# Kernel tuning notes

Hardware: AMD Instinct MI355X
Metric: run time of the kernel (lower is better)

Reference implementation:

```python
import jax, jax.numpy as jnp
import numpy as np

N_POWER_ITERS = 10  # torch spectral_norm power-iteration approximation of sigma_max

def _spectral_normalize(W):
    # Power iteration for largest singular value; u, v are treated as constants
    # w.r.t. gradients (matches torch.nn.utils.parametrizations.spectral_norm).
    u = jnp.ones((W.shape[0],), W.dtype) / jnp.sqrt(jnp.asarray(W.shape[0], W.dtype))
    def body(u, _):
        v = W.T @ u
        v = v / (jnp.linalg.norm(v) + 1e-12)
        u = W @ v
        u = u / (jnp.linalg.norm(u) + 1e-12)
        return u, None
    u, _ = jax.lax.scan(body, u, None, length=N_POWER_ITERS)
    u = jax.lax.stop_gradient(u)
    v = W.T @ u
    v = jax.lax.stop_gradient(v / (jnp.linalg.norm(v) + 1e-12))
    sigma = u @ (W @ v)
    return W / sigma

def setup_inputs() -> dict:
    key = jax.random.key(0)
    k1, k2, k3, k4 = jax.random.split(key, 4)
    B, T, D_in, H, D_out = 32, 1024, 1024, 1024, 1024
    x = jax.random.normal(k1, (B, T, D_in), dtype=jnp.float32)
    # nn.Linear weight shape: [out_features, in_features]
    W_A = jax.random.normal(k2, (H, H), dtype=jnp.float32) * (1.0 / np.sqrt(H))
    W_B = jax.random.normal(k3, (H, D_in), dtype=jnp.float32) * (1.0 / np.sqrt(D_in))
    W_C = jax.random.normal(k4, (D_out, H), dtype=jnp.float32) * (1.0 / np.sqrt(H))
    return {"x": x, "W_A": W_A, "W_B": W_B, "W_C": W_C}

def reference(x, W_A, W_B, W_C):
    A = _spectral_normalize(W_A)   # [H, H]
    Bw = _spectral_normalize(W_B)  # [H, D_in]
    C = _spectral_normalize(W_C)   # [D_out, H]
    # Precompute input projection for all timesteps: [B, T, H]
    xb = jnp.einsum('bti,hi->bth', x, Bw)
    h0 = jnp.zeros((x.shape[0], A.shape[0]), x.dtype)
    def step(h, xb_t):
        h = h @ A.T + xb_t   # h_t = A h_{t-1} + B x_t
        return h, h
    _, hs = jax.lax.scan(step, h0, jnp.swapaxes(xb, 0, 1))  # [T, B, H]
    hs = jnp.swapaxes(hs, 0, 1)                              # [B, T, H]
    ys = jnp.einsum('bth,oh->bto', hs, C)                    # y_t = C h_t
    return ys, hs
```

## Files before the change

kernel.cpp:

```cpp
#include <hip/hip_runtime.h>
#include <hip/hip_fp16.h>
#include <stdint.h>
#include <math.h>


typedef unsigned short us;
typedef float  floatx4 __attribute__((ext_vector_type(4)));
typedef short  shortx8 __attribute__((ext_vector_type(8)));

#define HDIM 1024
#define MALL 32768

__device__ __forceinline__ us f2bf(float f) {
  union { float f; unsigned u; } v; v.f = f;
  unsigned u = v.u;
  return (us)((u + 0x7FFFu + ((u >> 16) & 1u)) >> 16);
}
__device__ __forceinline__ float bf2f(us h) {
  union { float f; unsigned u; } v; v.u = ((unsigned)h) << 16;
  return v.f;
}

__device__ __forceinline__ void gbar(int* bar, int idx) {
  __threadfence();
  __syncthreads();
  if (threadIdx.x == 0) {
    __hip_atomic_fetch_add(&bar[idx], 1, __ATOMIC_ACQ_REL, __HIP_MEMORY_SCOPE_AGENT);
    while (__hip_atomic_load(&bar[idx], __ATOMIC_ACQUIRE, __HIP_MEMORY_SCOPE_AGENT) < 8)
      __builtin_amdgcn_s_sleep(2);
  }
  __syncthreads();
}

__global__ void k_power(const float* __restrict__ WA, const float* __restrict__ WB,
                        const float* __restrict__ WC,
                        float* __restrict__ uu, float* __restrict__ vv,
                        float* __restrict__ rsig, int* __restrict__ bar) {
  const int m = blockIdx.y, b = blockIdx.x, tid = threadIdx.x;
  const float* W = m == 0 ? WA : (m == 1 ? WB : WC);
  float* um = uu + m * 1024;
  float* vm = vv + m * 1024;
  int* barm = bar + m * 32;
  __shared__ float red[1024];
  __shared__ float vs[1024];

  if (tid < 128) um[b * 128 + tid] = 0.03125f;
  gbar(barm, 0);

  auto ssq_of = [&](const float* p) -> float {
    float a = p[tid];
    red[tid] = a * a; __syncthreads();
    for (int o = 512; o > 0; o >>= 1) { if (tid < o) red[tid] += red[tid + o]; __syncthreads(); }
    float r = red[0]; __syncthreads();
    return r;
  };

  const int il = tid & 127, jp = tid >> 7;
  const int jr = tid >> 3, ip = tid & 7;

  for (int it = 0; it <= 10; ++it) {
    float su = rsqrtf(ssq_of(um) + 1e-24f);
    {
      int i = b * 128 + il;
      float acc = 0.f;
      const float* Wp = W + (size_t)(jp * 128) * 1024 + i;
      #pragma unroll 4
      for (int j = 0; j < 128; ++j) acc = fmaf(Wp[(size_t)j * 1024], um[jp * 128 + j], acc);
      red[tid] = acc; __syncthreads();
      if (tid < 128) {
        float s = red[il] + red[il + 128] + red[il + 256] + red[il + 384]
                + red[il + 512] + red[il + 640] + red[il + 768] + red[il + 896];
        vm[b * 128 + il] = s * su;
      }
      __syncthreads();
    }
    gbar(barm, 1 + 2 * it);
    if (it == 10) break;
    float sv = rsqrtf(ssq_of(vm) + 1e-24f);
    vs[tid] = vm[tid] * sv;
    __syncthreads();
    {
      int j = b * 128 + jr;
      const float* Wr = W + (size_t)j * 1024;
      float acc = 0.f;
      #pragma unroll 4
      for (int k = 0; k < 128; ++k) acc = fmaf(Wr[ip + 8 * k], vs[ip + 8 * k], acc);
      #pragma unroll
      for (int o = 4; o > 0; o >>= 1) acc += __shfl_down(acc, o, 8);
      if (ip == 0) um[j] = acc;
    }
    __syncthreads();
    gbar(barm, 2 + 2 * it);
  }
  if (b == 0) {
    float s = ssq_of(vm);
    if (tid == 0) rsig[m] = rsqrtf(s + 1e-24f);
  }
}

__global__ void k_cast_mats(const float* __restrict__ WA, const float* __restrict__ WB,
                            const float* __restrict__ WC, const float* __restrict__ rsig,
                            us* __restrict__ dst) {
  int idx = blockIdx.x * 256 + threadIdx.x;
  if (idx >= 786432) return;
  int m = idx >> 18;
  const float* W = m == 0 ? WA : (m == 1 ? WB : WC);
  float rs = rsig[m];
  float4 v = ((const float4*)W)[idx & 262143];
  unsigned lo = f2bf(v.x * rs) | ((unsigned)f2bf(v.y * rs) << 16);
  unsigned hi = f2bf(v.z * rs) | ((unsigned)f2bf(v.w * rs) << 16);
  ((uint2*)dst)[idx] = make_uint2(lo, hi);
}

__global__ void k_cast_x(const float* __restrict__ src, us* __restrict__ dst, int n4) {
  int idx = blockIdx.x * 256 + threadIdx.x;
  int stride = gridDim.x * 256;
  for (; idx < n4; idx += stride) {
    float4 v = ((const float4*)src)[idx];
    unsigned lo = f2bf(v.x) | ((unsigned)f2bf(v.y) << 16);
    unsigned hi = f2bf(v.z) | ((unsigned)f2bf(v.w) << 16);
    ((uint2*)dst)[idx] = make_uint2(lo, hi);
  }
}

__global__ void k_transpose(const us* __restrict__ src, us* __restrict__ dst) {
  __shared__ us t[32][33];
  int bx = blockIdx.x * 32, by = blockIdx.y * 32;
  int tx = threadIdx.x & 31, ty = threadIdx.x >> 5;
  for (int r = ty; r < 32; r += 8)
    t[r][tx] = src[(size_t)(by + r) * 1024 + bx + tx];
  __syncthreads();
  for (int r = ty; r < 32; r += 8)
    dst[(size_t)(bx + r) * 1024 + by + tx] = t[tx][r];
}

template <int TILE>
__global__ __launch_bounds__(256, 3)
void k_gemm(const us* __restrict__ Abf, const us* __restrict__ Bmat,
            const us* __restrict__ AccP,
            float* __restrict__ Out32, us* __restrict__ Out16, us* __restrict__ OutH,
            us* __restrict__ Copy16,
            int M, int stride_log, int delta_a, int delta_acc, int delta_copy,
            int accmode, int zero_aop) {
  constexpr int BK = 64;
  constexpr int WT = TILE / 2;
  constexpr int NT = WT / 16;
  constexpr int QA = TILE / 32;

  __shared__ us ldsA[TILE * BK];
  __shared__ us ldsB[TILE * BK];

  const int tid = threadIdx.x;
  const int wave = tid >> 6, lane = tid & 63;
  const int wr = wave >> 1, wc = wave & 1;
  const int lr = lane & 15, g = lane >> 4;
  const int m0 = blockIdx.x * TILE, n0 = blockIdx.y * TILE;

  const int cnt_log = 10 - stride_log;
  const int cnt_mask = (1 << cnt_log) - 1;
  auto rowC = [&](int m) -> int {
    int j = m & cnt_mask, b = m >> cnt_log;
    return (b << 10) + (((j + 1) << stride_log) - 1);
  };

  floatx4 acc[NT][NT];
  if (accmode == 0) {
    #pragma unroll
    for (int i = 0; i < NT; ++i)
      #pragma unroll
      for (int j = 0; j < NT; ++j) acc[i][j] = (floatx4)(0.0f);
  } else {
    #pragma unroll
    for (int ii = 0; ii < NT; ++ii) {
      #pragma unroll
      for (int r = 0; r < 4; ++r) {
        int m = m0 + wr * WT + ii * 16 + g * 4 + r;
        if (m >= M) m = M - 1;
        size_t rowoff = (size_t)(rowC(m) - delta_acc) * HDIM;
        #pragma unroll
        for (int jj = 0; jj < NT; ++jj) {
          int col = n0 + wc * WT + jj * 16 + lr;
          us raw = AccP[rowoff + col];
          acc[ii][jj][r] = (accmode == 2) ? bf2f(raw)
                                          : __half2float(*(const __half*)&raw);
        }
      }
    }
  }

  if (!zero_aop) {
    size_t abase[QA], bbase[QA];
    #pragma unroll
    for (int q = 0; q < QA; ++q) {
      int ch = tid + q * 256;
      int i = ch >> 3;
      int c = (ch & 7) ^ ((i >> 1) & 7);
      int m = m0 + i; if (m >= M) m = M - 1;
      abase[q] = (size_t)(rowC(m) - delta_a) * HDIM + c * 8;
      bbase[q] = (size_t)(n0 + i) * HDIM + c * 8;
    }
    for (int k0 = 0; k0 < HDIM; k0 += BK) {
      __syncthreads();
      #pragma unroll
      for (int q = 0; q < QA; ++q) {
        __builtin_amdgcn_global_load_lds(
            (const __attribute__((address_space(1))) void*)(Abf + abase[q] + k0),
            (__attribute__((address_space(3))) void*)(ldsA + (wave * 64 + q * 256) * 8),
            16, 0, 0);
        __builtin_amdgcn_global_load_lds(
            (const __attribute__((address_space(1))) void*)(Bmat + bbase[q] + k0),
            (__attribute__((address_space(3))) void*)(ldsB + (wave * 64 + q * 256) * 8),
            16, 0, 0);
      }
      __syncthreads();
      #pragma unroll
      for (int kk = 0; kk < 2; ++kk) {
        shortx8 af[NT], bfv[NT];
        #pragma unroll
        for (int ii = 0; ii < NT; ++ii) {
          int ra = wr * WT + ii * 16 + lr;
          af[ii] = *(const shortx8*)(ldsA + ra * BK + (((kk * 4 + g) ^ ((ra >> 1) & 7)) * 8));
          int rb = wc * WT + ii * 16 + lr;
          bfv[ii] = *(const shortx8*)(ldsB + rb * BK + (((kk * 4 + g) ^ ((rb >> 1) & 7)) * 8));
        }
        #pragma unroll
        for (int ii = 0; ii < NT; ++ii)
          #pragma unroll
          for (int jj = 0; jj < NT; ++jj)
            acc[ii][jj] = __builtin_amdgcn_mfma_f32_16x16x32_bf16(af[ii], bfv[jj], acc[ii][jj], 0, 0, 0);
      }
    }
  }

  #pragma unroll
  for (int ii = 0; ii < NT; ++ii) {
    #pragma unroll
    for (int r = 0; r < 4; ++r) {
      int m = m0 + wr * WT + ii * 16 + g * 4 + r;
      if (m >= M) continue;
      size_t rowoff = (size_t)rowC(m) * HDIM;
      #pragma unroll
      for (int jj = 0; jj < NT; ++jj) {
        int col = n0 + wc * WT + jj * 16 + lr;
        float v = acc[ii][jj][r];
        if (Copy16) {
          us pv = zero_aop ? (us)0 : Abf[rowoff + col];
          Copy16[(size_t)(rowC(m) - delta_copy) * HDIM + col] = pv;
        }
        if (Out32) Out32[rowoff + col] = v;
        if (Out16) Out16[rowoff + col] = f2bf(v);
        if (OutH) {
          __half hv = __float2half(v);
          OutH[rowoff + col] = *(const us*)&hv;
        }
      }
    }
  }
}

extern "C" void kernel_launch(void* const* d_in, const int* in_sizes, int n_in,
                              void* d_out, int out_size, void* d_ws, size_t ws_size,
                              hipStream_t stream) {
  const float* x  = (const float*)d_in[0];
  const float* WA = (const float*)d_in[1];
  const float* WB = (const float*)d_in[2];
  const float* WC = (const float*)d_in[3];

  float* ys = (float*)d_out;
  float* U  = ys + (size_t)MALL * HDIM;
  us* U16 = (us*)U;

  char* wsb = (char*)d_ws;
  int*   bar  = (int*)(wsb);
  float* rsig = (float*)(wsb + 2048);
  float* uu   = (float*)(wsb + 4096);
  float* vv   = (float*)(wsb + 20480);
  us* An = (us*)(wsb + 65536);
  us* Bn = An + 1048576;
  us* Cn = Bn + 1048576;
  us* PT = Cn + 1048576;
  us* Ppow[9];
  Ppow[0] = An;
  for (int d = 1; d <= 8; ++d) Ppow[d] = PT + (size_t)d * 1048576;
  us* Xbf  = (us*)(wsb + 25231360);
  us* Uh   = Xbf;
  us* U0bf = Xbf + (size_t)MALL * HDIM;
  us* Ubf  = U0bf + (size_t)MALL * HDIM;
  if (ws_size < 226643968ULL) return;

  auto gemm = [&](int tile, const us* A, const us* B, const us* accP,
                  float* o32, us* o16, us* oH, us* cp16,
                  int M, int slog, int da, int dacc, int dcp, int am, int za) {
    dim3 grid((M + tile - 1) / tile, HDIM / tile);
    if (tile == 128)
      k_gemm<128><<<grid, 256, 0, stream>>>(A, B, accP, o32, o16, oH, cp16, M, slog, da, dacc, dcp, am, za);
    else
      k_gemm<64><<<grid, 256, 0, stream>>>(A, B, accP, o32, o16, oH, cp16, M, slog, da, dacc, dcp, am, za);
  };

  hipMemsetAsync(bar, 0, 3 * 32 * sizeof(int), stream);
  k_power<<<dim3(8, 3), 1024, 0, stream>>>(WA, WB, WC, uu, vv, rsig, bar);

  k_cast_mats<<<dim3(3072), 256, 0, stream>>>(WA, WB, WC, rsig, An);
  k_cast_x<<<dim3(8192), 256, 0, stream>>>(x, Xbf, 8388608);

  for (int d = 1; d <= 8; ++d) {
    k_transpose<<<dim3(32, 32), 256, 0, stream>>>(Ppow[d - 1], PT);
    gemm(64, Ppow[d - 1], PT, nullptr, nullptr, Ppow[d], nullptr, nullptr,
         1024, 0, 0, 0, 0, 0, 0);
  }

  gemm(128, Xbf, Bn, nullptr, nullptr, U0bf, nullptr, nullptr, MALL, 0, 0, 0, 0, 0, 0);

  for (int d = 0; d <= 8; ++d) {
    int M = MALL >> (d + 1);
    const us* srcA = (d == 0) ? U0bf : Ubf;
    const us* accP = (d == 0) ? U0bf : Uh;
    int am = (d == 0) ? 2 : 3;
    gemm(M >= 2048 ? 128 : 64, srcA, Ppow[d], accP, nullptr, Ubf, Uh, nullptr,
         M, d + 1, 1 << d, 0, 0, am, 0);
  }

  {
    us* PP2[2] = {U16, Ubf};
    for (int idx = 0; idx <= 9; ++idx) {
      int d = 9 - idx;
      int M = MALL >> (d + 1);
      const us* srcA = idx ? PP2[(idx - 1) & 1] : nullptr;
      us* dst = PP2[idx & 1];
      const us* accP = (d == 0) ? U0bf : Uh;
      int am = (d == 0) ? 2 : 3;
      gemm(M >= 2048 ? 128 : 64, srcA, Ppow[d], accP,
           nullptr, dst, nullptr, dst,
           M, d + 1, 0, 1 << d, 1 << d, am, idx == 0 ? 1 : 0);
    }
  }

  gemm(128, Ubf, An, U0bf, U, U0bf, nullptr, nullptr, MALL, 0, 0, 0, 0, 2, 0);

  gemm(128, U0bf, Cn, nullptr, ys, nullptr, nullptr, nullptr, MALL, 0, 0, 0, 0, 0, 0);
}
```

Before: 1.553 ms.

## Spread power iteration over more blocks with partial-norm reductions

```diff
diff --git a/kernel.cpp b/kernel.cpp
--- a/kernel.cpp
+++ b/kernel.cpp
@@ -10,6 +10,7 @@
 
 #define HDIM 1024
 #define MALL 32768
+#define PNB  32
 
 __device__ __forceinline__ us f2bf(float f) {
   union { float f; unsigned u; } v; v.f = f;
@@ -19,6 +20,12 @@
 __device__ __forceinline__ float bf2f(us h) {
   union { float f; unsigned u; } v; v.u = ((unsigned)h) << 16;
   return v.f;
+}
+
+__device__ __forceinline__ float bsum32(float t) {
+  #pragma unroll
+  for (int o = 16; o > 0; o >>= 1) t += __shfl_xor(t, o, 32);
+  return t;
 }
 
 __device__ __forceinline__ void gbar(int* bar, int idx) {
@@ -26,7 +33,7 @@
   __syncthreads();
   if (threadIdx.x == 0) {
     __hip_atomic_fetch_add(&bar[idx], 1, __ATOMIC_ACQ_REL, __HIP_MEMORY_SCOPE_AGENT);
-    while (__hip_atomic_load(&bar[idx], __ATOMIC_ACQUIRE, __HIP_MEMORY_SCOPE_AGENT) < 8)
+    while (__hip_atomic_load(&bar[idx], __ATOMIC_ACQUIRE, __HIP_MEMORY_SCOPE_AGENT) < PNB)
       __builtin_amdgcn_s_sleep(2);
   }
   __syncthreads();
@@ -35,77 +42,124 @@
 __global__ void k_power(const float* __restrict__ WA, const float* __restrict__ WB,
                         const float* __restrict__ WC,
                         float* __restrict__ uu, float* __restrict__ vv,
-                        float* __restrict__ rsig, int* __restrict__ bar) {
+                        float* __restrict__ part, int* __restrict__ bar) {
   const int m = blockIdx.y, b = blockIdx.x, tid = threadIdx.x;
   const float* W = m == 0 ? WA : (m == 1 ? WB : WC);
   float* um = uu + m * 1024;
   float* vm = vv + m * 1024;
-  int* barm = bar + m * 32;
-  __shared__ float red[1024];
-  __shared__ float vs[1024];
-
-  if (tid < 128) um[b * 128 + tid] = 0.03125f;
-  gbar(barm, 0);
-
-  auto ssq_of = [&](const float* p) -> float {
-    float a = p[tid];
-    red[tid] = a * a; __syncthreads();
-    for (int o = 512; o > 0; o >>= 1) { if (tid < o) red[tid] += red[tid + o]; __syncthreads(); }
-    float r = red[0]; __syncthreads();
-    return r;
-  };
-
-  const int il = tid & 127, jp = tid >> 7;
-  const int jr = tid >> 3, ip = tid & 7;
+  float* PV = part + m * 1024;
+  float* PU = part + m * 1024 + 512;
+  int* barm = bar + m * 64;
+
+  __shared__ __align__(16) float sh[1024];
+  __shared__ __align__(16) float red[512];
+  __shared__ float bc;
+
+  const int il = tid & 31, jp = tid >> 5;
+  const int jr = tid >> 4, ip = tid & 15;
 
   for (int it = 0; it <= 10; ++it) {
-    float su = rsqrtf(ssq_of(um) + 1e-24f);
+    if (it == 0) {
+      ((float2*)sh)[tid] = make_float2(0.03125f, 0.03125f);
+      __syncthreads();
+    } else {
+      if (tid < 32) {
+        float t = bsum32(PU[(it - 1) * 32 + tid]);
+        if (tid == 0) bc = rsqrtf(t + 1e-24f);
+      }
+      __syncthreads();
+      float su = bc;
+      float2 u2 = ((const float2*)um)[tid];
+      ((float2*)sh)[tid] = make_float2(u2.x * su, u2.y * su);
+      __syncthreads();
+    }
+
     {
-      int i = b * 128 + il;
-      float acc = 0.f;
-      const float* Wp = W + (size_t)(jp * 128) * 1024 + i;
-      #pragma unroll 4
-      for (int j = 0; j < 128; ++j) acc = fmaf(Wp[(size_t)j * 1024], um[jp * 128 + j], acc);
-      red[tid] = acc; __syncthreads();
-      if (tid < 128) {
-        float s = red[il] + red[il + 128] + red[il + 256] + red[il + 384]
-                + red[il + 512] + red[il + 640] + red[il + 768] + red[il + 896];
-        vm[b * 128 + il] = s * su;
-      }
-      __syncthreads();
-    }
-    gbar(barm, 1 + 2 * it);
+      const int col = b * 32 + il;
+      const float* Wp = W + (size_t)(jp * 64) * 1024 + col;
+      const float* up = sh + jp * 64;
+      float a0 = 0.f, a1 = 0.f, a2 = 0.f, a3 = 0.f, a4 = 0.f, a5 = 0.f, a6 = 0.f, a7 = 0.f;
+      #pragma unroll
+      for (int j = 0; j < 64; j += 8) {
+        a0 = fmaf(Wp[(size_t)(j + 0) * 1024], up[j + 0], a0);
+        a1 = fmaf(Wp[(size_t)(j + 1) * 1024], up[j + 1], a1);
+        a2 = fmaf(Wp[(size_t)(j + 2) * 1024], up[j + 2], a2);
+        a3 = fmaf(Wp[(size_t)(j + 3) * 1024], up[j + 3], a3);
+        a4 = fmaf(Wp[(size_t)(j + 4) * 1024], up[j + 4], a4);
+        a5 = fmaf(Wp[(size_t)(j + 5) * 1024], up[j + 5], a5);
+        a6 = fmaf(Wp[(size_t)(j + 6) * 1024], up[j + 6], a6);
+        a7 = fmaf(Wp[(size_t)(j + 7) * 1024], up[j + 7], a7);
+      }
+      red[tid] = ((a0 + a1) + (a2 + a3)) + ((a4 + a5) + (a6 + a7));
+      __syncthreads();
+      if (tid < 32) {
+        float s = 0.f;
+        #pragma unroll
+        for (int g = 0; g < 16; ++g) s += red[tid + 32 * g];
+        vm[b * 32 + tid] = s;
+        float t = bsum32(s * s);
+        if (tid == 0) PV[it * 32 + b] = t;
+      }
+    }
     if (it == 10) break;
-    float sv = rsqrtf(ssq_of(vm) + 1e-24f);
-    vs[tid] = vm[tid] * sv;
+    gbar(barm, 2 * it);
+
+    if (tid < 32) {
+      float t = bsum32(PV[it * 32 + tid]);
+      if (tid == 0) bc = rsqrtf(t + 1e-24f);
+    }
     __syncthreads();
     {
-      int j = b * 128 + jr;
-      const float* Wr = W + (size_t)j * 1024;
-      float acc = 0.f;
-      #pragma unroll 4
-      for (int k = 0; k < 128; ++k) acc = fmaf(Wr[ip + 8 * k], vs[ip + 8 * k], acc);
-      #pragma unroll
-      for (int o = 4; o > 0; o >>= 1) acc += __shfl_down(acc, o, 8);
-      if (ip == 0) um[j] = acc;
+      float sv = bc;
+      float2 v2 = ((const float2*)vm)[tid];
+      ((float2*)sh)[tid] = make_float2(v2.x * sv, v2.y * sv);
     }
     __syncthreads();
-    gbar(barm, 2 + 2 * it);
-  }
-  if (b == 0) {
-    float s = ssq_of(vm);
-    if (tid == 0) rsig[m] = rsqrtf(s + 1e-24f);
+
+    {
+      const int row = b * 32 + jr;
+      const float* Wr = W + (size_t)row * 1024;
+      float b0 = 0.f, b1 = 0.f, b2 = 0.f, b3 = 0.f, b4 = 0.f, b5 = 0.f, b6 = 0.f, b7 = 0.f;
+      #pragma unroll
+      for (int k = 0; k < 64; k += 8) {
+        b0 = fmaf(Wr[ip + 16 * (k + 0)], sh[ip + 16 * (k + 0)], b0);
+        b1 = fmaf(Wr[ip + 16 * (k + 1)], sh[ip + 16 * (k + 1)], b1);
+        b2 = fmaf(Wr[ip + 16 * (k + 2)], sh[ip + 16 * (k + 2)], b2);
+        b3 = fmaf(Wr[ip + 16 * (k + 3)], sh[ip + 16 * (k + 3)], b3);
+        b4 = fmaf(Wr[ip + 16 * (k + 4)], sh[ip + 16 * (k + 4)], b4);
+        b5 = fmaf(Wr[ip + 16 * (k + 5)], sh[ip + 16 * (k + 5)], b5);
+        b6 = fmaf(Wr[ip + 16 * (k + 6)], sh[ip + 16 * (k + 6)], b6);
+        b7 = fmaf(Wr[ip + 16 * (k + 7)], sh[ip + 16 * (k + 7)], b7);
+      }
+      float acc = ((b0 + b1) + (b2 + b3)) + ((b4 + b5) + (b6 + b7));
+      acc += __shfl_down(acc, 8, 16);
+      acc += __shfl_down(acc, 4, 16);
+      acc += __shfl_down(acc, 2, 16);
+      acc += __shfl_down(acc, 1, 16);
+      if (ip == 0) { um[row] = acc; red[jr] = acc * acc; }
+      __syncthreads();
+      if (tid < 32) {
+        float t = bsum32(red[tid]);
+        if (tid == 0) PU[it * 32 + b] = t;
+      }
+    }
+    gbar(barm, 2 * it + 1);
   }
 }
 
 __global__ void k_cast_mats(const float* __restrict__ WA, const float* __restrict__ WB,
-                            const float* __restrict__ WC, const float* __restrict__ rsig,
+                            const float* __restrict__ WC, const float* __restrict__ part,
                             us* __restrict__ dst) {
+  __shared__ float bcs;
+  const int m = (int)(((unsigned)blockIdx.x * 256u) >> 18);
+  if (threadIdx.x < 32) {
+    float t = bsum32(part[m * 1024 + 10 * 32 + threadIdx.x]);
+    if (threadIdx.x == 0) bcs = rsqrtf(t + 1e-24f);
+  }
+  __syncthreads();
+  float rs = bcs;
   int idx = blockIdx.x * 256 + threadIdx.x;
-  if (idx >= 786432) return;
-  int m = idx >> 18;
   const float* W = m == 0 ? WA : (m == 1 ? WB : WC);
-  float rs = rsig[m];
   float4 v = ((const float4*)W)[idx & 262143];
   unsigned lo = f2bf(v.x * rs) | ((unsigned)f2bf(v.y * rs) << 16);
   unsigned hi = f2bf(v.z * rs) | ((unsigned)f2bf(v.w * rs) << 16);
@@ -272,9 +326,9 @@
 
   char* wsb = (char*)d_ws;
   int*   bar  = (int*)(wsb);
-  float* rsig = (float*)(wsb + 2048);
   float* uu   = (float*)(wsb + 4096);
   float* vv   = (float*)(wsb + 20480);
+  float* part = (float*)(wsb + 32768);
   us* An = (us*)(wsb + 65536);
   us* Bn = An + 1048576;
   us* Cn = Bn + 1048576;
@@ -298,10 +352,10 @@
       k_gemm<64><<<grid, 256, 0, stream>>>(A, B, accP, o32, o16, oH, cp16, M, slog, da, dacc, dcp, am, za);
   };
 
-  hipMemsetAsync(bar, 0, 3 * 32 * sizeof(int), stream);
-  k_power<<<dim3(8, 3), 1024, 0, stream>>>(WA, WB, WC, uu, vv, rsig, bar);
-
-  k_cast_mats<<<dim3(3072), 256, 0, stream>>>(WA, WB, WC, rsig, An);
+  hipMemsetAsync(bar, 0, 3 * 64 * sizeof(int), stream);
+  k_power<<<dim3(PNB, 3), 512, 0, stream>>>(WA, WB, WC, uu, vv, part, bar);
+
+  k_cast_mats<<<dim3(3072), 256, 0, stream>>>(WA, WB, WC, part, An);
   k_cast_x<<<dim3(8192), 256, 0, stream>>>(x, Xbf, 8388608);
 
   for (int d = 1; d <= 8; ++d) {
```

After: 1.575 ms. No clear change (+1.4%).
